# Kernel optimization log

Hardware: AMD Instinct MI355X
Metric: run time of the kernel (lower is better)

## Reference

```python
import jax, jax.numpy as jnp
import numpy as np

B, N, D, K = 8, 2048, 512, 16


def setup_inputs() -> dict:
    key = jax.random.key(0)
    k1, k2, k3, k4, k5 = jax.random.split(key, 5)
    s = 1.0 / np.sqrt(D)
    return {
        "x": jax.random.normal(k1, (B, N, D), dtype=jnp.float32),
        "attn_w": jax.random.uniform(k2, (K, D), jnp.float32, -s, s),
        "attn_b": jax.random.uniform(k3, (K,), jnp.float32, -s, s),
        "w_merged": jax.random.uniform(k4, (D, D), jnp.float32, -s, s),
        "w_orig": jax.random.uniform(k5, (D, D), jnp.float32, -s, s),
    }


def reference(x, attn_w, attn_b, w_merged, w_orig):
    b, n, d = x.shape
    k = attn_w.shape[0]
    # cosine similarity matrix [B,N,N]
    xn = x / jnp.linalg.norm(x, axis=2, keepdims=True)
    w = jnp.einsum('bnd,bmd->bnm', xn, xn)
    # top-k neighbours per row
    _, idx = jax.lax.top_k(w, k)  # [B,N,K]
    bi = jnp.arange(b)[:, None, None]
    ni = jnp.arange(n)[None, :, None]
    # scatter 1s at top-k positions, then symmetrize (mutual-knn mask)
    mask = jnp.zeros((b, n, n), x.dtype).at[bi, ni, idx].set(1.0)
    mask = mask * jnp.swapaxes(mask, 1, 2)
    # learned per-neighbour attention logits scattered into dense [B,N,N]
    attn = x @ attn_w.T + attn_b  # [B,N,K]
    attn_full = jnp.zeros((b, n, n), x.dtype).at[bi, ni, idx].set(attn)
    scores = attn_full * mask + (-1e9) * (1.0 - mask)
    adj = jax.nn.softmax(scores, axis=2)
    # weighted aggregation + two projections
    merged = jnp.einsum('bnm,bmd->bnd', adj, x)
    out = jax.nn.relu(merged @ w_merged.T) + x @ w_orig.T
    return out
```

## Files before the change

kernel.cpp:

```cpp
#include <hip/hip_runtime.h>
#include <math.h>


#define NTOK 2048
#define DIM 512

typedef __attribute__((ext_vector_type(8))) __bf16 bf16x8;
typedef __attribute__((ext_vector_type(4))) float f32x4;
typedef __attribute__((ext_vector_type(8))) unsigned short ushort8;

#define GLDS(gp, lp)                                                      \
  __builtin_amdgcn_global_load_lds(                                       \
      (const __attribute__((address_space(1))) void*)(gp),                \
      (__attribute__((address_space(3))) void*)(lp), 16, 0, 0)

__device__ __forceinline__ ushort f2b(float f) {
  unsigned u = __float_as_uint(f);
  return (ushort)((u + 0x7fffu + ((u >> 16) & 1u)) >> 16);
}
__device__ __forceinline__ float b2f(ushort h) {
  return __uint_as_float((unsigned)h << 16);
}
__device__ __forceinline__ ushort f2key(float v) {
  union { _Float16 h; ushort u; } cv;
  cv.h = (_Float16)v;
  ushort hb = cv.u;
  return (hb & 0x8000u) ? (ushort)~hb : (ushort)(hb | 0x8000u);
}

__global__ __launch_bounds__(64) void k_norm(const float* __restrict__ x,
                                             const float* __restrict__ aw,
                                             const float* __restrict__ ab,
                                             ushort* __restrict__ xnb,
                                             ushort* __restrict__ xb,
                                             double* __restrict__ inv64,
                                             float* __restrict__ L) {
  int row = blockIdx.x, lane = threadIdx.x;
  const float* xr = x + (size_t)row * DIM;
  float4 a = *(const float4*)&xr[lane * 8];
  float4 b = *(const float4*)&xr[lane * 8 + 4];

  float s[16];
#pragma unroll
  for (int k = 0; k < 16; ++k) {
    const float4 w0 = *(const float4*)&aw[(size_t)k * DIM + lane * 8];
    const float4 w1 = *(const float4*)&aw[(size_t)k * DIM + lane * 8 + 4];
    s[k] = a.x * w0.x + a.y * w0.y + a.z * w0.z + a.w * w0.w + b.x * w1.x +
           b.y * w1.y + b.z * w1.z + b.w * w1.w;
  }
#pragma unroll
  for (int off = 1; off < 64; off <<= 1)
#pragma unroll
    for (int k = 0; k < 16; ++k) s[k] += __shfl_xor(s[k], off);

  double ss = (double)a.x * a.x + (double)a.y * a.y + (double)a.z * a.z +
              (double)a.w * a.w + (double)b.x * b.x + (double)b.y * b.y +
              (double)b.z * b.z + (double)b.w * b.w;
#pragma unroll
  for (int off = 32; off >= 1; off >>= 1) ss += __shfl_xor(ss, off);
  double inv = 1.0 / sqrt(ss);
  if (lane == 0) {
    inv64[row] = inv;
#pragma unroll
    for (int k = 0; k < 16; ++k) L[(size_t)row * 16 + k] = s[k] + ab[k];
  }
  float f = (float)inv;
  size_t o = (size_t)row * DIM + lane * 8;
  ushort4 r0 = {f2b(a.x), f2b(a.y), f2b(a.z), f2b(a.w)};
  ushort4 r1 = {f2b(b.x), f2b(b.y), f2b(b.z), f2b(b.w)};
  *(ushort4*)&xb[o] = r0;
  *(ushort4*)&xb[o + 4] = r1;
  ushort4 n0 = {f2b(a.x * f), f2b(a.y * f), f2b(a.z * f), f2b(a.w * f)};
  ushort4 n1 = {f2b(b.x * f), f2b(b.y * f), f2b(b.z * f), f2b(b.w * f)};
  *(ushort4*)&xnb[o] = n0;
  *(ushort4*)&xnb[o + 4] = n1;
}

__global__ __launch_bounds__(256) void k_castw(const float* __restrict__ a,
                                               const float* __restrict__ b,
                                               ushort* __restrict__ ab,
                                               ushort* __restrict__ bb) {
  int i = (blockIdx.x * 256 + threadIdx.x) * 4;
  float4 va = *(const float4*)&a[i];
  float4 vb = *(const float4*)&b[i];
  ushort4 oa = {f2b(va.x), f2b(va.y), f2b(va.z), f2b(va.w)};
  ushort4 ob = {f2b(vb.x), f2b(vb.y), f2b(vb.z), f2b(vb.w)};
  *(ushort4*)&ab[i] = oa;
  *(ushort4*)&bb[i] = ob;
}

__device__ __forceinline__ void bt_kloop(const ushort* __restrict__ A,
                                         const ushort* __restrict__ B,
                                         ushort* lA, ushort* lB, int rb, int cb,
                                         int tid, f32x4 (&acc)[4][4]) {
  int wv = tid >> 6, ln = tid & 63;
  int wm = wv >> 1, wn = wv & 1;
  int col = ln & 15, quad = ln >> 4;
  for (int kt = 0; kt < DIM; kt += 32) {
#pragma unroll
    for (int j = 0; j < 2; ++j) {
      int c = j * 256 + wv * 64 + ln;
      int r = c >> 2, seg = c & 3;
      GLDS(A + (size_t)(rb + r) * DIM + kt + seg * 8, lA + c * 8);
      GLDS(B + (size_t)(cb + r) * DIM + kt + seg * 8, lB + c * 8);
    }
    __syncthreads();
    bf16x8 af[4], bf[4];
#pragma unroll
    for (int i = 0; i < 4; ++i) {
      af[i] = *(const bf16x8*)&lA[(wm * 64 + i * 16 + col) * 32 + quad * 8];
      bf[i] = *(const bf16x8*)&lB[(wn * 64 + i * 16 + col) * 32 + quad * 8];
    }
#pragma unroll
    for (int i = 0; i < 4; ++i)
#pragma unroll
      for (int j = 0; j < 4; ++j)
        acc[i][j] =
            __builtin_amdgcn_mfma_f32_16x16x32_bf16(af[i], bf[j], acc[i][j], 0, 0, 0);
    __syncthreads();
  }
}

__global__ __launch_bounds__(256) void k_simgemm(const ushort* __restrict__ Xn,
                                                 ushort* __restrict__ Skey) {
  __shared__ ushort lA[128 * 32];
  __shared__ ushort lB[128 * 32];
  __shared__ ushort st[128 * 136];
  int tid = threadIdx.x;
  int z = blockIdx.z;
  const ushort* Xb = Xn + (size_t)z * NTOK * DIM;
  ushort* Sb = Skey + (size_t)z * NTOK * NTOK;
  int ti = 0, rem = blockIdx.x;
  while (rem >= 16 - ti) { rem -= 16 - ti; ++ti; }
  int tj = ti + rem;
  int rb = ti * 128, cb = tj * 128;
  f32x4 zero = {0.f, 0.f, 0.f, 0.f};
  f32x4 acc[4][4];
#pragma unroll
  for (int i = 0; i < 4; ++i)
#pragma unroll
    for (int j = 0; j < 4; ++j) acc[i][j] = zero;
  bt_kloop(Xb, Xb, lA, lB, rb, cb, tid, acc);
  int wv = tid >> 6, ln = tid & 63;
  int wm = wv >> 1, wn = wv & 1;
  int col = ln & 15, quad = ln >> 4;
#pragma unroll
  for (int i = 0; i < 4; ++i)
#pragma unroll
    for (int j = 0; j < 4; ++j) {
      int r0 = wm * 64 + i * 16 + quad * 4;
      int c = wn * 64 + j * 16 + col;
      ushort4 kk = {f2key(acc[i][j][0]), f2key(acc[i][j][1]),
                    f2key(acc[i][j][2]), f2key(acc[i][j][3])};
      *(ushort4*)&Sb[(size_t)(cb + c) * NTOK + rb + r0] = kk;
      st[(r0 + 0) * 136 + c] = kk.x;
      st[(r0 + 1) * 136 + c] = kk.y;
      st[(r0 + 2) * 136 + c] = kk.z;
      st[(r0 + 3) * 136 + c] = kk.w;
    }
  __syncthreads();
#pragma unroll
  for (int p = 0; p < 8; ++p) {
    int r = p * 16 + (tid >> 4);
    int cs = (tid & 15) * 8;
    ushort8 row = *(const ushort8*)&st[r * 136 + cs];
    *(ushort8*)&Sb[(size_t)(rb + r) * NTOK + cb + cs] = row;
  }
}

__global__ __launch_bounds__(256) void k_proj(const ushort* __restrict__ Mg,
                                              const ushort* __restrict__ Wm,
                                              const ushort* __restrict__ Xg,
                                              const ushort* __restrict__ Wo,
                                              float* __restrict__ out) {
  __shared__ ushort lA[128 * 32];
  __shared__ ushort lB[128 * 32];
  int tid = threadIdx.x;
  int rb = blockIdx.x * 128, cb = blockIdx.y * 128;
  f32x4 zero = {0.f, 0.f, 0.f, 0.f};
  f32x4 a1[4][4], a2[4][4];
#pragma unroll
  for (int i = 0; i < 4; ++i)
#pragma unroll
    for (int j = 0; j < 4; ++j) { a1[i][j] = zero; a2[i][j] = zero; }
  bt_kloop(Mg, Wm, lA, lB, rb, cb, tid, a1);
  bt_kloop(Xg, Wo, lA, lB, rb, cb, tid, a2);
  int wv = tid >> 6, ln = tid & 63;
  int wm = wv >> 1, wn = wv & 1;
  int col = ln & 15, quad = ln >> 4;
#pragma unroll
  for (int i = 0; i < 4; ++i)
#pragma unroll
    for (int j = 0; j < 4; ++j)
#pragma unroll
      for (int r = 0; r < 4; ++r) {
        int m = rb + wm * 64 + i * 16 + quad * 4 + r;
        int n = cb + wn * 64 + j * 16 + col;
        out[(size_t)m * DIM + n] = fmaxf(a1[i][j][r], 0.f) + a2[i][j][r];
      }
}

#define TARGET 24

__device__ __forceinline__ void scan_pick(const unsigned* hist, int lane,
                                          int tgt, int* out_v,
                                          unsigned* out_cntv1) {
  int base = lane * 4;
  unsigned h0 = hist[0 * 256 + base + 0] + hist[1 * 256 + base + 0] +
                hist[2 * 256 + base + 0] + hist[3 * 256 + base + 0];
  unsigned h1 = hist[0 * 256 + base + 1] + hist[1 * 256 + base + 1] +
                hist[2 * 256 + base + 1] + hist[3 * 256 + base + 1];
  unsigned h2 = hist[0 * 256 + base + 2] + hist[1 * 256 + base + 2] +
                hist[2 * 256 + base + 2] + hist[3 * 256 + base + 2];
  unsigned h3 = hist[0 * 256 + base + 3] + hist[1 * 256 + base + 3] +
                hist[2 * 256 + base + 3] + hist[3 * 256 + base + 3];
  unsigned s3 = h3, s2 = h2 + s3, s1 = h1 + s2, s0 = h0 + s1;
  unsigned inc = s0;
#pragma unroll
  for (int off = 1; off < 64; off <<= 1) {
    unsigned o = __shfl_down(inc, off);
    if (lane + off < 64) inc += o;
  }
  unsigned above = inc - s0;
  int vb = -1;
  if (above + s0 >= (unsigned)tgt) vb = base + 0;
  if (above + s1 >= (unsigned)tgt) vb = base + 1;
  if (above + s2 >= (unsigned)tgt) vb = base + 2;
  if (above + s3 >= (unsigned)tgt) vb = base + 3;
  int v = vb;
#pragma unroll
  for (int off = 1; off < 64; off <<= 1) v = max(v, __shfl_xor(v, off));
  unsigned v1 = 0;
  if ((v >> 2) == lane) {
    int k = v & 3;
    v1 = (k == 0) ? above + s1 : (k == 1) ? above + s2
                               : (k == 2) ? above + s3 : above;
  }
  v1 = __shfl(v1, v >> 2);
  *out_v = v;
  *out_cntv1 = v1;
}

__global__ __launch_bounds__(256) void k_topk(const ushort* __restrict__ simk,
                                              const float* __restrict__ x,
                                              const double* __restrict__ inv64,
                                              int* __restrict__ idx16,
                                              int batch0, int pbm1, int pbsh) {
  int zi = blockIdx.x & pbm1;
  int n = blockIdx.x >> pbsh;
  int batch = batch0 + zi;
  int t = threadIdx.x;
  int wave = t >> 6, lane = t & 63;
  __shared__ unsigned hist[4 * 256];
  __shared__ int lidx[32];
  __shared__ double vals[32];
  __shared__ int shv, sneed, sthr, lcnt;
  const ushort* srow = simk + ((size_t)zi * NTOK + (size_t)n) * NTOK;

  const float* xrow = x + ((size_t)batch * NTOK + n) * DIM;
  float4 xa0 = *(const float4*)&xrow[lane * 8];
  float4 xa1 = *(const float4*)&xrow[lane * 8 + 4];
  double dinvn = inv64[(size_t)batch * NTOK + n];

  ushort kv[8];
  {
    ushort8 v8 = *(const ushort8*)&srow[t * 8];
#pragma unroll
    for (int e = 0; e < 8; ++e) kv[e] = v8[e];
  }
#pragma unroll
  for (int i = 0; i < 4; ++i) hist[t + 256 * i] = 0;
  if (t == 0) lcnt = 0;
  __syncthreads();
#pragma unroll
  for (int j = 0; j < 8; ++j)
    atomicAdd(&hist[wave * 256 + (kv[j] >> 8)], 1u);
  __syncthreads();
  if (wave == 0) {
    int v;
    unsigned v1;
    scan_pick(hist, lane, TARGET, &v, &v1);
    if (lane == 0) { shv = v; sneed = TARGET - (int)v1; }
  }
  __syncthreads();
  int v = shv;
#pragma unroll
  for (int i = 0; i < 4; ++i) hist[t + 256 * i] = 0;
  __syncthreads();
#pragma unroll
  for (int j = 0; j < 8; ++j)
    if ((kv[j] >> 8) == v) atomicAdd(&hist[wave * 256 + (kv[j] & 255)], 1u);
  __syncthreads();
  if (wave == 0) {
    int u;
    unsigned dummy;
    scan_pick(hist, lane, sneed, &u, &dummy);
    if (lane == 0) sthr = (v << 8) | u;
  }
  __syncthreads();
  unsigned thr = (unsigned)sthr;
#pragma unroll
  for (int j = 0; j < 8; ++j) {
    if ((unsigned)kv[j] >= thr) {
      int slot = atomicAdd(&lcnt, 1);
      if (slot < 32) lidx[slot] = t * 8 + j;
    }
  }
  __syncthreads();
  int c = lcnt < 32 ? lcnt : 32;
  for (int s = wave; s < c; s += 4) {
    int m = lidx[s];
    const float* xc = x + ((size_t)batch * NTOK + m) * DIM;
    float4 b0 = *(const float4*)&xc[lane * 8];
    float4 b1 = *(const float4*)&xc[lane * 8 + 4];
    double sacc = 0.0;
    sacc = fma((double)xa0.x, (double)b0.x, sacc);
    sacc = fma((double)xa0.y, (double)b0.y, sacc);
    sacc = fma((double)xa0.z, (double)b0.z, sacc);
    sacc = fma((double)xa0.w, (double)b0.w, sacc);
    sacc = fma((double)xa1.x, (double)b1.x, sacc);
    sacc = fma((double)xa1.y, (double)b1.y, sacc);
    sacc = fma((double)xa1.z, (double)b1.z, sacc);
    sacc = fma((double)xa1.w, (double)b1.w, sacc);
#pragma unroll
    for (int off = 1; off < 64; off <<= 1) sacc += __shfl_xor(sacc, off);
    if (lane == 0)
      vals[s] = sacc * dinvn * inv64[(size_t)batch * NTOK + m];
  }
  __syncthreads();
  if (t < 32) {
    double sv = (t < c) ? vals[t] : -1.0e300;
    int si = (t < c) ? lidx[t] : 0x7FFFFFFF;
#pragma unroll
    for (int k = 2; k <= 32; k <<= 1) {
#pragma unroll
      for (int jj = k >> 1; jj > 0; jj >>= 1) {
        double ov = __shfl_xor(sv, jj);
        int oi = __shfl_xor(si, jj);
        bool lower = (t & jj) == 0;
        bool desc = (t & k) == 0;
        bool takeFirst = (lower == desc);
        bool otherFirst = (ov > sv) || (ov == sv && oi < si);
        if (takeFirst == otherFirst) { sv = ov; si = oi; }
      }
    }
    if (t < 16) idx16[((size_t)batch * NTOK + n) * 16 + t] = si;
  }
}

__global__ __launch_bounds__(128) void k_merge(const ushort* __restrict__ xb,
                                               const int* __restrict__ idx16,
                                               const float* __restrict__ L,
                                               ushort* __restrict__ mergedb) {
  int b = blockIdx.x & 7;
  int n = blockIdx.x >> 3;
  int row = (b << 11) | n;
  int t = threadIdx.x;
  __shared__ float ps[16];
  __shared__ int ms[16];
  if (t < 64) {
    int k = t & 15;
    int m = idx16[(size_t)row * 16 + k];
    const int* mrow = idx16 + (size_t)(b * NTOK + m) * 16;
    int4 q0 = *(const int4*)&mrow[0];
    int4 q1 = *(const int4*)&mrow[4];
    int4 q2 = *(const int4*)&mrow[8];
    int4 q3 = *(const int4*)&mrow[12];
    bool mut = (q0.x == n) | (q0.y == n) | (q0.z == n) | (q0.w == n) |
               (q1.x == n) | (q1.y == n) | (q1.z == n) | (q1.w == n) |
               (q2.x == n) | (q2.y == n) | (q2.z == n) | (q2.w == n) |
               (q3.x == n) | (q3.y == n) | (q3.z == n) | (q3.w == n);
    float l = mut ? L[(size_t)row * 16 + k] : -__builtin_inff();
    float mx = l;
#pragma unroll
    for (int off = 1; off < 16; off <<= 1) mx = fmaxf(mx, __shfl_xor(mx, off));
    float e = mut ? __expf(l - mx) : 0.0f;
    float den = e;
#pragma unroll
    for (int off = 1; off < 16; off <<= 1) den += __shfl_xor(den, off);
    if (t < 16) { ps[t] = e / den; ms[t] = m; }
  }
  __syncthreads();
  float4 acc = {0.f, 0.f, 0.f, 0.f};
#pragma unroll
  for (int k = 0; k < 16; ++k) {
    float pk = ps[k];
    if (pk != 0.0f) {
      ushort4 v = *(const ushort4*)&xb[(size_t)(b * NTOK + ms[k]) * DIM + t * 4];
      acc.x = fmaf(pk, b2f(v.x), acc.x);
      acc.y = fmaf(pk, b2f(v.y), acc.y);
      acc.z = fmaf(pk, b2f(v.z), acc.z);
      acc.w = fmaf(pk, b2f(v.w), acc.w);
    }
  }
  ushort4 o = {f2b(acc.x), f2b(acc.y), f2b(acc.z), f2b(acc.w)};
  *(ushort4*)&mergedb[(size_t)row * DIM + t * 4] = o;
}

extern "C" void kernel_launch(void* const* d_in, const int* in_sizes, int n_in,
                              void* d_out, int out_size, void* d_ws,
                              size_t ws_size, hipStream_t stream) {
  const float* x = (const float*)d_in[0];
  const float* attn_w = (const float*)d_in[1];
  const float* attn_b = (const float*)d_in[2];
  const float* w_merged = (const float*)d_in[3];
  const float* w_orig = (const float*)d_in[4];
  float* out = (float*)d_out;

  char* w = (char*)d_ws;
  ushort* xnb = (ushort*)(w);
  ushort* xb = (ushort*)(w + 16777216);
  double* inv64 = (double*)(w + 33554432);
  ushort* wmb = (ushort*)(w + 33685504);
  ushort* wob = (ushort*)(w + 34209792);
  int* idx16 = (int*)(w + 34734080);
  float* L = (float*)(w + 35782656);
  ushort* simk = (ushort*)(w + 36831232);
  ushort* mergedb = (ushort*)(w + 36831232);

  size_t fixed = 36831232ull, per = 8388608ull;
  int pb = 1, pbsh = 0;
  if (ws_size >= fixed + 8 * per) { pb = 8; pbsh = 3; }
  else if (ws_size >= fixed + 4 * per) { pb = 4; pbsh = 2; }
  else if (ws_size >= fixed + 2 * per) { pb = 2; pbsh = 1; }

  k_norm<<<16384, 64, 0, stream>>>(x, attn_w, attn_b, xnb, xb, inv64, L);
  k_castw<<<256, 256, 0, stream>>>(w_merged, w_orig, wmb, wob);
  for (int b = 0; b < 8; b += pb) {
    k_simgemm<<<dim3(136, 1, pb), 256, 0, stream>>>(
        xnb + (size_t)b * NTOK * DIM, simk);
    k_topk<<<NTOK * pb, 256, 0, stream>>>(simk, x, inv64, idx16, b, pb - 1,
                                          pbsh);
  }
  k_merge<<<16384, 128, 0, stream>>>(xb, idx16, L, mergedb);
  k_proj<<<dim3(128, 4), 256, 0, stream>>>(mergedb, wmb, xb, wob, out);
}
```

Measured before the change: 303.1 us.

## Double-buffer LDS tiles in similarity and projection GEMMs

Replaces the load-sync-compute-sync K loop with a double-buffered pipeline: the next K-slice is issued via global_load_lds into the alternate buffer while MFMAs consume the current one, with one barrier per iteration. In k_simgemm the second buffer reuses the epilogue staging array. In k_proj the two GEMMs are interleaved in a single loop with four double-buffered tiles (64KB LDS), which may reduce occupancy.

```diff
diff --git a/kernel.cpp b/kernel.cpp
--- a/kernel.cpp
+++ b/kernel.cpp
@@ -89,43 +89,43 @@
   *(ushort4*)&bb[i] = ob;
 }
 
-__device__ __forceinline__ void bt_kloop(const ushort* __restrict__ A,
-                                         const ushort* __restrict__ B,
-                                         ushort* lA, ushort* lB, int rb, int cb,
-                                         int tid, f32x4 (&acc)[4][4]) {
-  int wv = tid >> 6, ln = tid & 63;
-  int wm = wv >> 1, wn = wv & 1;
-  int col = ln & 15, quad = ln >> 4;
-  for (int kt = 0; kt < DIM; kt += 32) {
-#pragma unroll
-    for (int j = 0; j < 2; ++j) {
-      int c = j * 256 + wv * 64 + ln;
-      int r = c >> 2, seg = c & 3;
-      GLDS(A + (size_t)(rb + r) * DIM + kt + seg * 8, lA + c * 8);
-      GLDS(B + (size_t)(cb + r) * DIM + kt + seg * 8, lB + c * 8);
-    }
-    __syncthreads();
-    bf16x8 af[4], bf[4];
-#pragma unroll
-    for (int i = 0; i < 4; ++i) {
-      af[i] = *(const bf16x8*)&lA[(wm * 64 + i * 16 + col) * 32 + quad * 8];
-      bf[i] = *(const bf16x8*)&lB[(wn * 64 + i * 16 + col) * 32 + quad * 8];
-    }
-#pragma unroll
-    for (int i = 0; i < 4; ++i)
-#pragma unroll
-      for (int j = 0; j < 4; ++j)
-        acc[i][j] =
-            __builtin_amdgcn_mfma_f32_16x16x32_bf16(af[i], bf[j], acc[i][j], 0, 0, 0);
-    __syncthreads();
-  }
+__device__ __forceinline__ void stage2(const ushort* __restrict__ A,
+                                       const ushort* __restrict__ B,
+                                       ushort* lA, ushort* lB, int rb, int cb,
+                                       int kt, int wv, int ln) {
+#pragma unroll
+  for (int j = 0; j < 2; ++j) {
+    int c = j * 256 + wv * 64 + ln;
+    int r = c >> 2, seg = c & 3;
+    GLDS(A + (size_t)(rb + r) * DIM + kt + seg * 8, lA + c * 8);
+    GLDS(B + (size_t)(cb + r) * DIM + kt + seg * 8, lB + c * 8);
+  }
+}
+
+__device__ __forceinline__ void frag_mfma(const ushort* lA, const ushort* lB,
+                                          int wm, int wn, int col, int quad,
+                                          f32x4 (&acc)[4][4]) {
+  bf16x8 af[4], bf[4];
+#pragma unroll
+  for (int i = 0; i < 4; ++i) {
+    af[i] = *(const bf16x8*)&lA[(wm * 64 + i * 16 + col) * 32 + quad * 8];
+    bf[i] = *(const bf16x8*)&lB[(wn * 64 + i * 16 + col) * 32 + quad * 8];
+  }
+#pragma unroll
+  for (int i = 0; i < 4; ++i)
+#pragma unroll
+    for (int j = 0; j < 4; ++j)
+      acc[i][j] =
+          __builtin_amdgcn_mfma_f32_16x16x32_bf16(af[i], bf[j], acc[i][j], 0, 0, 0);
 }
 
 __global__ __launch_bounds__(256) void k_simgemm(const ushort* __restrict__ Xn,
                                                  ushort* __restrict__ Skey) {
-  __shared__ ushort lA[128 * 32];
-  __shared__ ushort lB[128 * 32];
-  __shared__ ushort st[128 * 136];
+  __shared__ __align__(16) ushort lA0[128 * 32];
+  __shared__ __align__(16) ushort lB0[128 * 32];
+  __shared__ __align__(16) ushort st[128 * 136];
+  ushort* lA1 = st;
+  ushort* lB1 = st + 128 * 32;
   int tid = threadIdx.x;
   int z = blockIdx.z;
   const ushort* Xb = Xn + (size_t)z * NTOK * DIM;
@@ -134,16 +134,29 @@
   while (rem >= 16 - ti) { rem -= 16 - ti; ++ti; }
   int tj = ti + rem;
   int rb = ti * 128, cb = tj * 128;
-  f32x4 zero = {0.f, 0.f, 0.f, 0.f};
-  f32x4 acc[4][4];
-#pragma unroll
-  for (int i = 0; i < 4; ++i)
-#pragma unroll
-    for (int j = 0; j < 4; ++j) acc[i][j] = zero;
-  bt_kloop(Xb, Xb, lA, lB, rb, cb, tid, acc);
   int wv = tid >> 6, ln = tid & 63;
   int wm = wv >> 1, wn = wv & 1;
   int col = ln & 15, quad = ln >> 4;
+  f32x4 zero = {0.f, 0.f, 0.f, 0.f};
+  f32x4 acc[4][4];
+#pragma unroll
+  for (int i = 0; i < 4; ++i)
+#pragma unroll
+    for (int j = 0; j < 4; ++j) acc[i][j] = zero;
+
+  stage2(Xb, Xb, lA0, lB0, rb, cb, 0, wv, ln);
+  __syncthreads();
+#pragma unroll
+  for (int kt16 = 0; kt16 < 16; ++kt16) {
+    const ushort* cA = (kt16 & 1) ? lA1 : lA0;
+    const ushort* cB = (kt16 & 1) ? lB1 : lB0;
+    if (kt16 < 15)
+      stage2(Xb, Xb, (kt16 & 1) ? lA0 : lA1, (kt16 & 1) ? lB0 : lB1, rb, cb,
+             (kt16 + 1) * 32, wv, ln);
+    frag_mfma(cA, cB, wm, wn, col, quad, acc);
+    __syncthreads();
+  }
+
 #pragma unroll
   for (int i = 0; i < 4; ++i)
 #pragma unroll
@@ -173,21 +186,48 @@
                                               const ushort* __restrict__ Xg,
                                               const ushort* __restrict__ Wo,
                                               float* __restrict__ out) {
-  __shared__ ushort lA[128 * 32];
-  __shared__ ushort lB[128 * 32];
+  __shared__ __align__(16) ushort lds[32768];
+  ushort* A1a = lds;
+  ushort* B1a = lds + 4096;
+  ushort* A2a = lds + 8192;
+  ushort* B2a = lds + 12288;
+  ushort* A1b = lds + 16384;
+  ushort* B1b = lds + 20480;
+  ushort* A2b = lds + 24576;
+  ushort* B2b = lds + 28672;
   int tid = threadIdx.x;
   int rb = blockIdx.x * 128, cb = blockIdx.y * 128;
-  f32x4 zero = {0.f, 0.f, 0.f, 0.f};
-  f32x4 a1[4][4], a2[4][4];
-#pragma unroll
-  for (int i = 0; i < 4; ++i)
-#pragma unroll
-    for (int j = 0; j < 4; ++j) { a1[i][j] = zero; a2[i][j] = zero; }
-  bt_kloop(Mg, Wm, lA, lB, rb, cb, tid, a1);
-  bt_kloop(Xg, Wo, lA, lB, rb, cb, tid, a2);
   int wv = tid >> 6, ln = tid & 63;
   int wm = wv >> 1, wn = wv & 1;
   int col = ln & 15, quad = ln >> 4;
+  f32x4 zero = {0.f, 0.f, 0.f, 0.f};
+  f32x4 a1[4][4], a2[4][4];
+#pragma unroll
+  for (int i = 0; i < 4; ++i)
+#pragma unroll
+    for (int j = 0; j < 4; ++j) { a1[i][j] = zero; a2[i][j] = zero; }
+
+  stage2(Mg, Wm, A1a, B1a, rb, cb, 0, wv, ln);
+  stage2(Xg, Wo, A2a, B2a, rb, cb, 0, wv, ln);
+  __syncthreads();
+#pragma unroll
+  for (int kt16 = 0; kt16 < 16; ++kt16) {
+    const bool odd = kt16 & 1;
+    const ushort* cA1 = odd ? A1b : A1a;
+    const ushort* cB1 = odd ? B1b : B1a;
+    const ushort* cA2 = odd ? A2b : A2a;
+    const ushort* cB2 = odd ? B2b : B2a;
+    if (kt16 < 15) {
+      stage2(Mg, Wm, odd ? A1a : A1b, odd ? B1a : B1b, rb, cb,
+             (kt16 + 1) * 32, wv, ln);
+      stage2(Xg, Wo, odd ? A2a : A2b, odd ? B2a : B2b, rb, cb,
+             (kt16 + 1) * 32, wv, ln);
+    }
+    frag_mfma(cA1, cB1, wm, wn, col, quad, a1);
+    frag_mfma(cA2, cB2, wm, wn, col, quad, a2);
+    __syncthreads();
+  }
+
 #pragma unroll
   for (int i = 0; i < 4; ++i)
 #pragma unroll
```

Measured after the change: 301.1 us. No clear change (-0.7%).
